# Kernel tuning notes

Measured on AMD Instinct MI355X. Metric: run time of the kernel, lower is better.

The kernel has to match this reference:

```python
import jax, jax.numpy as jnp
import numpy as np

B, IN_C, W, H = 16, 1024, 32, 32
P = 256          # planes
HEADS = 4
D = P // HEADS   # 64
N = W * H
EPS = 1e-6


def setup_inputs() -> dict:
    key = jax.random.key(0)
    ks = jax.random.split(key, 12)
    s = lambda fan_in: 1.0 / np.sqrt(fan_in)
    return {
        "x": jax.random.normal(ks[0], (B, IN_C, W, H), jnp.float32),
        "w_ds": jax.random.normal(ks[1], (P, IN_C), jnp.float32) * s(IN_C),
        "wq": jax.random.normal(ks[2], (P, P), jnp.float32) * s(P),
        "bq": jax.random.normal(ks[3], (P,), jnp.float32) * 0.01,
        "wk": jax.random.normal(ks[4], (P, P), jnp.float32) * s(P),
        "bk": jax.random.normal(ks[5], (P,), jnp.float32) * 0.01,
        "wv": jax.random.normal(ks[6], (P, P), jnp.float32) * s(P),
        "bv": jax.random.normal(ks[7], (P,), jnp.float32) * 0.01,
        "rel_h": jax.random.normal(ks[8], (1, HEADS, D, 1, H), jnp.float32),
        "rel_w": jax.random.normal(ks[9], (1, HEADS, D, W, 1), jnp.float32),
        "ln_w": jnp.ones((P,), jnp.float32),
        "ln_b": jnp.zeros((P,), jnp.float32),
        "w1": jax.random.normal(ks[10], (IN_C, P), jnp.float32) * s(P),
    }


def _conv1x1(w, x, b=None):
    # w: [out, in], x: [B, in, W, H]
    y = jnp.einsum('oc,bchw->bohw', w, x)
    if b is not None:
        y = y + b[None, :, None, None]
    return y


def reference(x, w_ds, wq, bq, wk, bk, wv, bv, rel_h, rel_w, ln_w, ln_b, w1):
    out = _conv1x1(w_ds, x)  # [B, P, W, H]

    # --- MHSA ---
    q = _conv1x1(wq, out, bq).reshape(B, HEADS, D, N)
    k = _conv1x1(wk, out, bk).reshape(B, HEADS, D, N)
    v = _conv1x1(wv, out, bv).reshape(B, HEADS, D, N)

    content_content = jnp.einsum('bhdi,bhdj->bhij', q, k)  # q^T k
    pos = (rel_h + rel_w).reshape(1, HEADS, D, N)           # [1,h,d,N]
    # content_position[i,j] = pos_i . q_j  (faithful to original: matmul with q)
    content_position = jnp.einsum('xhdi,bhdj->bhij', pos, q)
    attn = jax.nn.softmax(content_content + content_position, axis=-1)
    # out[.., d, i] = sum_j v[.., d, j] * attn[.., i, j]
    o = jnp.einsum('bhdj,bhij->bhdi', v, attn).reshape(B, P, W, H)

    # --- LayerNorm (channels_last over channel dim) ---
    y = o.transpose(0, 2, 3, 1)  # [B, W, H, P]
    mu = y.mean(-1, keepdims=True)
    var = ((y - mu) ** 2).mean(-1, keepdims=True)
    y = (y - mu) / jnp.sqrt(var + EPS) * ln_w + ln_b
    y = y.transpose(0, 3, 1, 2)  # [B, P, W, H]

    # --- expand conv + exact GELU + residual ---
    out2 = jax.nn.gelu(_conv1x1(w1, y), approximate=False)
    return out2 + x
```

## Files before the change

### kernel.cpp

```cpp
#include <hip/hip_runtime.h>
#include <hip/hip_bf16.h>
#include <math.h>

#define NN 1024
#define PP 256
#define INC 1024

typedef _Float16 f16_t;
typedef __attribute__((ext_vector_type(8))) _Float16 f16x8;
typedef __attribute__((ext_vector_type(4))) _Float16 f16x4;
typedef __attribute__((ext_vector_type(4))) float f32x4;
typedef __attribute__((ext_vector_type(16))) float f32x16;
typedef __attribute__((ext_vector_type(4))) int i32x4;

__device__ __forceinline__ float gelu_exact(float v) {
    return 0.5f * v * (1.0f + erff(v * 0.70710678118654752440f));
}

__device__ __forceinline__ void cvt_store(const float* __restrict__ s,
                                          f16_t* __restrict__ d, int j) {
    float4 v = ((const float4*)s)[j];
    f16x4 o = {(f16_t)v.x, (f16_t)v.y, (f16_t)v.z, (f16_t)v.w};
    ((f16x4*)d)[j] = o;
}

__global__ __launch_bounds__(256) void prep_k(
    const float* __restrict__ w_ds, const float* __restrict__ wq,
    const float* __restrict__ wk, const float* __restrict__ wv,
    const float* __restrict__ w1, const float* __restrict__ rel_h,
    const float* __restrict__ rel_w, const float* __restrict__ bq,
    const float* __restrict__ bk, const float* __restrict__ bv,
    f16_t* __restrict__ wdsh, f16_t* __restrict__ wqkv,
    f16_t* __restrict__ w1h, f16_t* __restrict__ post,
    float* __restrict__ bqkv)
{
    int i = blockIdx.x * 256 + threadIdx.x;
    if (i < 65536) {
        cvt_store(w_ds, wdsh, i);
    } else if (i < 81920) {
        cvt_store(wq, wqkv, i - 65536);
    } else if (i < 98304) {
        cvt_store(wk, wqkv + 65536, i - 81920);
    } else if (i < 114688) {
        cvt_store(wv, wqkv + 131072, i - 98304);
    } else if (i < 180224) {
        cvt_store(w1, w1h, i - 114688);
    } else if (i < 245760) {
        int j = i - 180224;
        int flat = j * 4;
        int d = flat & 63;
        int n = (flat >> 6) & 1023;
        int h = flat >> 16;
        f16x4 pk;
        #pragma unroll
        for (int jj = 0; jj < 4; ++jj) {
            float v = rel_h[(h * 64 + d + jj) * 32 + (n & 31)]
                    + rel_w[(h * 64 + d + jj) * 32 + (n >> 5)];
            pk[jj] = (f16_t)v;
        }
        *(f16x4*)&post[flat] = pk;
    } else if (i < 245952) {
        int j = i - 245760;
        int which = j >> 6, r = j & 63;
        const float* src = which == 0 ? bq : (which == 1 ? bk : bv);
        float4 v = ((const float4*)src)[r];
        ((float4*)bqkv)[which * 64 + r] = v;
    }
}

__global__ __launch_bounds__(256) void transpose_xk(const float* __restrict__ x,
                                                    f16_t* __restrict__ xt) {
    __shared__ float T[64][68];
    int tid = threadIdx.x;
    int n0 = blockIdx.x * 64, c0 = blockIdx.y * 64;
    size_t b = blockIdx.z;
    const float* xp = x + b * 1048576;
    int cl = tid >> 4, n4 = (tid & 15) * 4;
    #pragma unroll
    for (int it = 0; it < 4; ++it) {
        float4 v = *(const float4*)&xp[(size_t)(c0 + cl + it * 16) * 1024 + n0 + n4];
        *(float4*)&T[cl + it * 16][n4] = v;
    }
    __syncthreads();
    int nl = tid >> 3, ck = tid & 7;
    f16_t* xo = xt + b * 1048576;
    #pragma unroll
    for (int it = 0; it < 2; ++it) {
        int n = nl + it * 32;
        f16x8 pk;
        #pragma unroll
        for (int j = 0; j < 8; ++j) pk[j] = (f16_t)T[ck * 8 + j][n];
        *(f16x8*)&xo[(size_t)(n0 + n) * 1024 + c0 + ck * 8] = pk;
    }
}

__global__ __launch_bounds__(64) void hgemm(
    const f16_t* __restrict__ A, const f16_t* __restrict__ Bt,
    const float* __restrict__ bias, const float* __restrict__ resid,
    f16_t* __restrict__ Cq, f16_t* __restrict__ Ck, f16_t* __restrict__ Cv,
    float* __restrict__ Cf,
    int M, int N, int K, int mode)
{
    int l = threadIdx.x;
    int lo = l & 15, hi = l >> 4;
    int m0 = blockIdx.y * 64;
    int n0 = blockIdx.x * 32;
    size_t bb = blockIdx.z;

    const f16_t* Ap = A + (size_t)(m0 + lo) * K + hi * 8;
    const f16_t* Bq = Bt + bb * (size_t)N * K + (size_t)(n0 + lo) * K + hi * 8;

    f32x4 acc[4][2] = {};

    #pragma unroll 2
    for (int k0 = 0; k0 < K; k0 += 32) {
        f16x8 bfr0 = *(const f16x8*)(Bq + k0);
        f16x8 bfr1 = *(const f16x8*)(Bq + (size_t)16 * K + k0);
        #pragma unroll
        for (int fm = 0; fm < 4; ++fm) {
            f16x8 af = *(const f16x8*)(Ap + (size_t)fm * 16 * K + k0);
            acc[fm][0] = __builtin_amdgcn_mfma_f32_16x16x32_f16(af, bfr0, acc[fm][0], 0, 0, 0);
            acc[fm][1] = __builtin_amdgcn_mfma_f32_16x16x32_f16(af, bfr1, acc[fm][1], 0, 0, 0);
        }
    }

    #pragma unroll
    for (int fn = 0; fn < 2; ++fn) {
        int n = n0 + fn * 16 + lo;
        #pragma unroll
        for (int fm = 0; fm < 4; ++fm) {
            int mb = m0 + fm * 16 + hi * 4;
            f32x4 a = acc[fm][fn];
            if (mode == 0) {
                f16x4 st;
                #pragma unroll
                for (int r = 0; r < 4; ++r) st[r] = (f16_t)a[r];
                *(f16x4*)&Cq[((size_t)bb * N + n) * M + mb] = st;
            } else if (mode == 1) {
                int which = mb >> 8;
                int mloc = mb & 255;
                int hh = mloc >> 6, d0 = mloc & 63;
                if (which == 2) {
                    #pragma unroll
                    for (int r = 0; r < 4; ++r)
                        Cv[(((size_t)bb * 4 + hh) * 64 + d0 + r) * NN + n] = (f16_t)(a[r] + bias[mb + r]);
                } else {
                    f16_t* dst = which ? Ck : Cq;
                    f16x4 st;
                    #pragma unroll
                    for (int r = 0; r < 4; ++r) st[r] = (f16_t)(a[r] + bias[mb + r]);
                    *(f16x4*)&dst[(((size_t)bb * 4 + hh) * NN + n) * 64 + d0] = st;
                }
            } else {
                #pragma unroll
                for (int r = 0; r < 4; ++r) {
                    size_t idx = ((size_t)bb * M + mb + r) * N + n;
                    Cf[idx] = gelu_exact(a[r]) + resid[idx];
                }
            }
        }
    }
}

__global__ __launch_bounds__(64) void attn_mfma(
    const f16_t* __restrict__ q_t, const f16_t* __restrict__ k_t,
    const f16_t* __restrict__ v_b, const f16_t* __restrict__ pos_t,
    f16_t* __restrict__ o)
{
    int l = threadIdx.x;
    int lq = l & 31;
    int half = l >> 5;
    int h = blockIdx.y, b = blockIdx.z;
    int q0 = blockIdx.x * 32;
    size_t base = (size_t)(b * 4 + h) * (NN * 64);

    f16x8 Bq0, Bq1, Bq2, Bq3, Bq4, Bq5, Bq6, Bq7;
    {
        const f16_t* qr = q_t + base + (size_t)(q0 + lq) * 64 + half * 8;
        Bq0 = *(const f16x8*)(qr);
        Bq1 = *(const f16x8*)(qr + 16);
        Bq2 = *(const f16x8*)(qr + 32);
        Bq3 = *(const f16x8*)(qr + 48);
        const f16_t* pr = pos_t + ((size_t)h * NN + q0 + lq) * 64 + half * 8;
        Bq4 = *(const f16x8*)(pr);
        Bq5 = *(const f16x8*)(pr + 16);
        Bq6 = *(const f16x8*)(pr + 32);
        Bq7 = *(const f16x8*)(pr + 48);
    }

    f32x16 accD0 = {}, accD1 = {};
    float m_run = -1e30f, l_run = 0.0f;

    const f16_t* kbase = k_t + base + (size_t)lq * 64 + half * 8;
    const f16_t* qbase = q_t + base + (size_t)lq * 64 + half * 8;
    const f16_t* vbase = v_b + base + (size_t)lq * NN + half * 8;

    f16x8 aK0, aK1, aK2, aK3, aQ0, aQ1, aQ2, aQ3, aV00, aV01, aV10, aV11;
    f16x8 bK0, bK1, bK2, bK3, bQ0, bQ1, bQ2, bQ3, bV00, bV01, bV10, bV11;

#define LOADT(S, J) do { \
    const f16_t* ka_ = kbase + (size_t)(J) * 64; \
    S##K0 = *(const f16x8*)(ka_);       S##K1 = *(const f16x8*)(ka_ + 16); \
    S##K2 = *(const f16x8*)(ka_ + 32);  S##K3 = *(const f16x8*)(ka_ + 48); \
    const f16_t* qa_ = qbase + (size_t)(J) * 64; \
    S##Q0 = *(const f16x8*)(qa_);       S##Q1 = *(const f16x8*)(qa_ + 16); \
    S##Q2 = *(const f16x8*)(qa_ + 32);  S##Q3 = *(const f16x8*)(qa_ + 48); \
    const f16_t* va_ = vbase + (J); \
    S##V00 = *(const f16x8*)(va_);          S##V01 = *(const f16x8*)(va_ + 16); \
    S##V10 = *(const f16x8*)(va_ + 32 * NN); S##V11 = *(const f16x8*)(va_ + 32 * NN + 16); \
} while (0)

#define COMPUTE(S) do { \
    f32x16 sc = {}; \
    sc = __builtin_amdgcn_mfma_f32_32x32x16_f16(S##K0, Bq0, sc, 0, 0, 0); \
    sc = __builtin_amdgcn_mfma_f32_32x32x16_f16(S##K1, Bq1, sc, 0, 0, 0); \
    sc = __builtin_amdgcn_mfma_f32_32x32x16_f16(S##K2, Bq2, sc, 0, 0, 0); \
    sc = __builtin_amdgcn_mfma_f32_32x32x16_f16(S##K3, Bq3, sc, 0, 0, 0); \
    sc = __builtin_amdgcn_mfma_f32_32x32x16_f16(S##Q0, Bq4, sc, 0, 0, 0); \
    sc = __builtin_amdgcn_mfma_f32_32x32x16_f16(S##Q1, Bq5, sc, 0, 0, 0); \
    sc = __builtin_amdgcn_mfma_f32_32x32x16_f16(S##Q2, Bq6, sc, 0, 0, 0); \
    sc = __builtin_amdgcn_mfma_f32_32x32x16_f16(S##Q3, Bq7, sc, 0, 0, 0); \
    float mt = sc[0]; \
    _Pragma("unroll") \
    for (int r = 1; r < 16; ++r) mt = fmaxf(mt, sc[r]); \
    mt = fmaxf(mt, __shfl_xor(mt, 32, 64)); \
    if (!__all(mt <= m_run + 8.0f)) { \
        float mnew = fmaxf(m_run, mt); \
        float alpha = __expf(m_run - mnew); \
        m_run = mnew; l_run *= alpha; \
        _Pragma("unroll") \
        for (int r = 0; r < 16; ++r) { accD0[r] *= alpha; accD1[r] *= alpha; } \
    } \
    float p[16]; float rs = 0.0f; \
    _Pragma("unroll") \
    for (int r = 0; r < 16; ++r) { p[r] = __expf(sc[r] - m_run); rs += p[r]; } \
    rs += __shfl_xor(rs, 32, 64); \
    l_run += rs; \
    int w0 = __builtin_bit_cast(int, __builtin_amdgcn_cvt_pkrtz(p[0], p[1])); \
    int w1 = __builtin_bit_cast(int, __builtin_amdgcn_cvt_pkrtz(p[2], p[3])); \
    int w2 = __builtin_bit_cast(int, __builtin_amdgcn_cvt_pkrtz(p[4], p[5])); \
    int w3 = __builtin_bit_cast(int, __builtin_amdgcn_cvt_pkrtz(p[6], p[7])); \
    int w4 = __builtin_bit_cast(int, __builtin_amdgcn_cvt_pkrtz(p[8], p[9])); \
    int w5 = __builtin_bit_cast(int, __builtin_amdgcn_cvt_pkrtz(p[10], p[11])); \
    int w6 = __builtin_bit_cast(int, __builtin_amdgcn_cvt_pkrtz(p[12], p[13])); \
    int w7 = __builtin_bit_cast(int, __builtin_amdgcn_cvt_pkrtz(p[14], p[15])); \
    int x0 = __shfl_xor(w0, 32, 64), x1 = __shfl_xor(w1, 32, 64); \
    int x2 = __shfl_xor(w2, 32, 64), x3 = __shfl_xor(w3, 32, 64); \
    int x4 = __shfl_xor(w4, 32, 64), x5 = __shfl_xor(w5, 32, 64); \
    int x6 = __shfl_xor(w6, 32, 64), x7 = __shfl_xor(w7, 32, 64); \
    i32x4 pb0 = { half ? x2 : w0, half ? x3 : w1, half ? w2 : x0, half ? w3 : x1 }; \
    i32x4 pb1 = { half ? x6 : w4, half ? x7 : w5, half ? w6 : x4, half ? w7 : x5 }; \
    f16x8 Pf0 = __builtin_bit_cast(f16x8, pb0); \
    f16x8 Pf1 = __builtin_bit_cast(f16x8, pb1); \
    accD0 = __builtin_amdgcn_mfma_f32_32x32x16_f16(S##V00, Pf0, accD0, 0, 0, 0); \
    accD0 = __builtin_amdgcn_mfma_f32_32x32x16_f16(S##V01, Pf1, accD0, 0, 0, 0); \
    accD1 = __builtin_amdgcn_mfma_f32_32x32x16_f16(S##V10, Pf0, accD1, 0, 0, 0); \
    accD1 = __builtin_amdgcn_mfma_f32_32x32x16_f16(S##V11, Pf1, accD1, 0, 0, 0); \
} while (0)

    LOADT(a, 0);
    for (int t = 0; t < 32; t += 2) {
        LOADT(b, (t + 1) * 32);
        COMPUTE(a);
        LOADT(a, (size_t)(((t + 2) & 31) * 32));
        COMPUTE(b);
    }
#undef LOADT
#undef COMPUTE

    float inv = 1.0f / l_run;
    size_t orow = ((size_t)b * NN + q0 + lq) * 256 + h * 64;
    #pragma unroll
    for (int rg = 0; rg < 4; ++rg) {
        f16x4 s0, s1;
        #pragma unroll
        for (int c = 0; c < 4; ++c) {
            s0[c] = (f16_t)(accD0[rg * 4 + c] * inv);
            s1[c] = (f16_t)(accD1[rg * 4 + c] * inv);
        }
        *(f16x4*)&o[orow + rg * 8 + half * 4] = s0;
        *(f16x4*)&o[orow + 32 + rg * 8 + half * 4] = s1;
    }
}

__global__ __launch_bounds__(256) void ln_k(const f16_t* __restrict__ o,
                                            f16_t* __restrict__ yt,
                                            const float* __restrict__ lw,
                                            const float* __restrict__ lb)
{
    int tid = threadIdx.x;
    int wv = tid >> 6, l = tid & 63;
    size_t row = (size_t)blockIdx.x * 4 + wv;
    f16x4 v4 = ((const f16x4*)(o + row * 256))[l];
    float v[4];
    #pragma unroll
    for (int j = 0; j < 4; ++j) v[j] = (float)v4[j];
    float s = v[0] + v[1] + v[2] + v[3];
    float q = v[0]*v[0] + v[1]*v[1] + v[2]*v[2] + v[3]*v[3];
    #pragma unroll
    for (int off = 1; off < 64; off <<= 1) {
        s += __shfl_xor(s, off, 64);
        q += __shfl_xor(q, off, 64);
    }
    float mean = s * (1.0f / 256.0f);
    float var = q * (1.0f / 256.0f) - mean * mean;
    float rstd = rsqrtf(var + 1e-6f);
    f32x4 w4 = ((const f32x4*)lw)[l];
    f32x4 b4 = ((const f32x4*)lb)[l];
    f16x4 o4;
    #pragma unroll
    for (int j = 0; j < 4; ++j)
        o4[j] = (f16_t)((v[j] - mean) * rstd * w4[j] + b4[j]);
    ((f16x4*)(yt + row * 256))[l] = o4;
}

extern "C" void kernel_launch(void* const* d_in, const int* in_sizes, int n_in,
                              void* d_out, int out_size, void* d_ws, size_t ws_size,
                              hipStream_t stream) {
    const float* x     = (const float*)d_in[0];
    const float* w_ds  = (const float*)d_in[1];
    const float* wq    = (const float*)d_in[2];
    const float* bq    = (const float*)d_in[3];
    const float* wk    = (const float*)d_in[4];
    const float* bk    = (const float*)d_in[5];
    const float* wv    = (const float*)d_in[6];
    const float* bv    = (const float*)d_in[7];
    const float* rel_h = (const float*)d_in[8];
    const float* rel_w = (const float*)d_in[9];
    const float* ln_w  = (const float*)d_in[10];
    const float* ln_b  = (const float*)d_in[11];
    const float* w1    = (const float*)d_in[12];
    float* out = (float*)d_out;

    f16_t* xt    = (f16_t*)d_ws;
    f16_t* wdsh  = xt + 16777216;
    f16_t* wqkv  = wdsh + 262144;
    f16_t* w1h   = wqkv + 196608;
    f16_t* post  = w1h + 262144;
    f16_t* out0t = post + 262144;
    f16_t* qt    = out0t + 4194304;
    f16_t* kt    = qt + 4194304;
    f16_t* vb    = kt + 4194304;
    f16_t* ytb   = vb + 4194304;
    f16_t* oat   = ytb + 4194304;
    float* bqkv  = (float*)(oat + 4194304);

    prep_k<<<961, 256, 0, stream>>>(w_ds, wq, wk, wv, w1, rel_h, rel_w,
                                    bq, bk, bv, wdsh, wqkv, w1h, post, bqkv);
    transpose_xk<<<dim3(16, 16, 16), 256, 0, stream>>>(x, xt);

    hgemm<<<dim3(32, 4, 16), 64, 0, stream>>>(wdsh, xt, nullptr, nullptr,
                                              out0t, nullptr, nullptr, nullptr,
                                              PP, NN, INC, 0);
    hgemm<<<dim3(32, 12, 16), 64, 0, stream>>>(wqkv, out0t, bqkv, nullptr,
                                               qt, kt, vb, nullptr,
                                               768, NN, PP, 1);
    attn_mfma<<<dim3(32, 4, 16), 64, 0, stream>>>(qt, kt, vb, post, oat);
    ln_k<<<4096, 256, 0, stream>>>(oat, ytb, ln_w, ln_b);
    hgemm<<<dim3(32, 16, 16), 64, 0, stream>>>(w1h, ytb, nullptr, x,
                                               nullptr, nullptr, nullptr, out,
                                               INC, NN, PP, 3);
}
```

Baseline: 396.6 us.

## Split attention KV range across four waves and shrink GEMM M-tiles

The attention kernel now runs four waves per block. Each wave processes a quarter of the key/value sequence, and the partial softmax statistics and accumulators are merged through shared memory with a log-sum-exp rescale before one wave writes the output. This gives each block more parallelism and shortens the serial KV loop. The GEMM kernel is templated on M-fragment count, and the first two GEMMs use smaller M-tiles to launch more blocks. The cost is extra synchronisation and shared-memory traffic in attention, and less A/B reuse per block in the GEMMs.

New measurement: 529.3 us. +33.5%, slower.

```diff
diff --git a/kernel.cpp b/kernel.cpp
--- a/kernel.cpp
+++ b/kernel.cpp
@@ -94,6 +94,7 @@
     }
 }
 
+template<int MFR>
 __global__ __launch_bounds__(64) void hgemm(
     const f16_t* __restrict__ A, const f16_t* __restrict__ Bt,
     const float* __restrict__ bias, const float* __restrict__ resid,
@@ -103,21 +104,21 @@
 {
     int l = threadIdx.x;
     int lo = l & 15, hi = l >> 4;
-    int m0 = blockIdx.y * 64;
+    int m0 = blockIdx.y * (MFR * 16);
     int n0 = blockIdx.x * 32;
     size_t bb = blockIdx.z;
 
     const f16_t* Ap = A + (size_t)(m0 + lo) * K + hi * 8;
     const f16_t* Bq = Bt + bb * (size_t)N * K + (size_t)(n0 + lo) * K + hi * 8;
 
-    f32x4 acc[4][2] = {};
+    f32x4 acc[MFR][2] = {};
 
     #pragma unroll 2
     for (int k0 = 0; k0 < K; k0 += 32) {
         f16x8 bfr0 = *(const f16x8*)(Bq + k0);
         f16x8 bfr1 = *(const f16x8*)(Bq + (size_t)16 * K + k0);
         #pragma unroll
-        for (int fm = 0; fm < 4; ++fm) {
+        for (int fm = 0; fm < MFR; ++fm) {
             f16x8 af = *(const f16x8*)(Ap + (size_t)fm * 16 * K + k0);
             acc[fm][0] = __builtin_amdgcn_mfma_f32_16x16x32_f16(af, bfr0, acc[fm][0], 0, 0, 0);
             acc[fm][1] = __builtin_amdgcn_mfma_f32_16x16x32_f16(af, bfr1, acc[fm][1], 0, 0, 0);
@@ -128,7 +129,7 @@
     for (int fn = 0; fn < 2; ++fn) {
         int n = n0 + fn * 16 + lo;
         #pragma unroll
-        for (int fm = 0; fm < 4; ++fm) {
+        for (int fm = 0; fm < MFR; ++fm) {
             int mb = m0 + fm * 16 + hi * 4;
             f32x4 a = acc[fm][fn];
             if (mode == 0) {
@@ -162,12 +163,16 @@
     }
 }
 
-__global__ __launch_bounds__(64) void attn_mfma(
+__global__ __launch_bounds__(256, 4) void attn_mfma(
     const f16_t* __restrict__ q_t, const f16_t* __restrict__ k_t,
     const f16_t* __restrict__ v_b, const f16_t* __restrict__ pos_t,
     f16_t* __restrict__ o)
 {
-    int l = threadIdx.x;
+    __shared__ float cm[4][32], cl[4][32];
+    __shared__ __align__(16) float cacc[2][32][68];
+    int tid = threadIdx.x;
+    int wvi = tid >> 6;
+    int l = tid & 63;
     int lq = l & 31;
     int half = l >> 5;
     int h = blockIdx.y, b = blockIdx.z;
@@ -191,9 +196,9 @@
     f32x16 accD0 = {}, accD1 = {};
     float m_run = -1e30f, l_run = 0.0f;
 
-    const f16_t* kbase = k_t + base + (size_t)lq * 64 + half * 8;
-    const f16_t* qbase = q_t + base + (size_t)lq * 64 + half * 8;
-    const f16_t* vbase = v_b + base + (size_t)lq * NN + half * 8;
+    const f16_t* kbase = k_t + base + ((size_t)wvi * 256 + lq) * 64 + half * 8;
+    const f16_t* qabase = q_t + base + ((size_t)wvi * 256 + lq) * 64 + half * 8;
+    const f16_t* vbase = v_b + base + (size_t)lq * NN + wvi * 256 + half * 8;
 
     f16x8 aK0, aK1, aK2, aK3, aQ0, aQ1, aQ2, aQ3, aV00, aV01, aV10, aV11;
     f16x8 bK0, bK1, bK2, bK3, bQ0, bQ1, bQ2, bQ3, bV00, bV01, bV10, bV11;
@@ -202,7 +207,7 @@
     const f16_t* ka_ = kbase + (size_t)(J) * 64; \
     S##K0 = *(const f16x8*)(ka_);       S##K1 = *(const f16x8*)(ka_ + 16); \
     S##K2 = *(const f16x8*)(ka_ + 32);  S##K3 = *(const f16x8*)(ka_ + 48); \
-    const f16_t* qa_ = qbase + (size_t)(J) * 64; \
+    const f16_t* qa_ = qabase + (size_t)(J) * 64; \
     S##Q0 = *(const f16x8*)(qa_);       S##Q1 = *(const f16x8*)(qa_ + 16); \
     S##Q2 = *(const f16x8*)(qa_ + 32);  S##Q3 = *(const f16x8*)(qa_ + 48); \
     const f16_t* va_ = vbase + (J); \
@@ -259,27 +264,82 @@
 } while (0)
 
     LOADT(a, 0);
-    for (int t = 0; t < 32; t += 2) {
+    for (int t = 0; t < 8; t += 2) {
         LOADT(b, (t + 1) * 32);
         COMPUTE(a);
-        LOADT(a, (size_t)(((t + 2) & 31) * 32));
+        LOADT(a, ((t + 2) & 7) * 32);
         COMPUTE(b);
     }
 #undef LOADT
 #undef COMPUTE
 
-    float inv = 1.0f / l_run;
-    size_t orow = ((size_t)b * NN + q0 + lq) * 256 + h * 64;
-    #pragma unroll
-    for (int rg = 0; rg < 4; ++rg) {
-        f16x4 s0, s1;
-        #pragma unroll
-        for (int c = 0; c < 4; ++c) {
-            s0[c] = (f16_t)(accD0[rg * 4 + c] * inv);
-            s1[c] = (f16_t)(accD1[rg * 4 + c] * inv);
-        }
-        *(f16x4*)&o[orow + rg * 8 + half * 4] = s0;
-        *(f16x4*)&o[orow + 32 + rg * 8 + half * 4] = s1;
+    if (half == 0) { cm[wvi][lq] = m_run; cl[wvi][lq] = l_run; }
+    __syncthreads();
+    float m0v = cm[0][lq], m1v = cm[1][lq], m2v = cm[2][lq], m3v = cm[3][lq];
+    float mg = fmaxf(fmaxf(m0v, m1v), fmaxf(m2v, m3v));
+    float lg = cl[0][lq] * __expf(m0v - mg) + cl[1][lq] * __expf(m1v - mg)
+             + cl[2][lq] * __expf(m2v - mg) + cl[3][lq] * __expf(m3v - mg);
+    float alpha = __expf(m_run - mg);
+    #pragma unroll
+    for (int r = 0; r < 16; ++r) { accD0[r] *= alpha; accD1[r] *= alpha; }
+
+    if (wvi & 1) {
+        int bi = wvi >> 1;
+        #pragma unroll
+        for (int rg = 0; rg < 4; ++rg) {
+            int d0 = rg * 8 + half * 4;
+            float4 v0 = {accD0[rg*4+0], accD0[rg*4+1], accD0[rg*4+2], accD0[rg*4+3]};
+            float4 v1 = {accD1[rg*4+0], accD1[rg*4+1], accD1[rg*4+2], accD1[rg*4+3]};
+            *(float4*)&cacc[bi][lq][d0] = v0;
+            *(float4*)&cacc[bi][lq][32 + d0] = v1;
+        }
+    }
+    __syncthreads();
+    if (!(wvi & 1)) {
+        int bi = wvi >> 1;
+        #pragma unroll
+        for (int rg = 0; rg < 4; ++rg) {
+            int d0 = rg * 8 + half * 4;
+            float4 v0 = *(const float4*)&cacc[bi][lq][d0];
+            float4 v1 = *(const float4*)&cacc[bi][lq][32 + d0];
+            accD0[rg*4+0] += v0.x; accD0[rg*4+1] += v0.y; accD0[rg*4+2] += v0.z; accD0[rg*4+3] += v0.w;
+            accD1[rg*4+0] += v1.x; accD1[rg*4+1] += v1.y; accD1[rg*4+2] += v1.z; accD1[rg*4+3] += v1.w;
+        }
+    }
+    __syncthreads();
+    if (wvi == 2) {
+        #pragma unroll
+        for (int rg = 0; rg < 4; ++rg) {
+            int d0 = rg * 8 + half * 4;
+            float4 v0 = {accD0[rg*4+0], accD0[rg*4+1], accD0[rg*4+2], accD0[rg*4+3]};
+            float4 v1 = {accD1[rg*4+0], accD1[rg*4+1], accD1[rg*4+2], accD1[rg*4+3]};
+            *(float4*)&cacc[1][lq][d0] = v0;
+            *(float4*)&cacc[1][lq][32 + d0] = v1;
+        }
+    }
+    __syncthreads();
+    if (wvi == 0) {
+        #pragma unroll
+        for (int rg = 0; rg < 4; ++rg) {
+            int d0 = rg * 8 + half * 4;
+            float4 v0 = *(const float4*)&cacc[1][lq][d0];
+            float4 v1 = *(const float4*)&cacc[1][lq][32 + d0];
+            accD0[rg*4+0] += v0.x; accD0[rg*4+1] += v0.y; accD0[rg*4+2] += v0.z; accD0[rg*4+3] += v0.w;
+            accD1[rg*4+0] += v1.x; accD1[rg*4+1] += v1.y; accD1[rg*4+2] += v1.z; accD1[rg*4+3] += v1.w;
+        }
+        float inv = 1.0f / lg;
+        size_t orow = ((size_t)b * NN + q0 + lq) * 256 + h * 64;
+        #pragma unroll
+        for (int rg = 0; rg < 4; ++rg) {
+            f16x4 s0, s1;
+            #pragma unroll
+            for (int c = 0; c < 4; ++c) {
+                s0[c] = (f16_t)(accD0[rg * 4 + c] * inv);
+                s1[c] = (f16_t)(accD1[rg * 4 + c] * inv);
+            }
+            *(f16x4*)&o[orow + rg * 8 + half * 4] = s0;
+            *(f16x4*)&o[orow + 32 + rg * 8 + half * 4] = s1;
+        }
     }
 }
 
@@ -349,15 +409,15 @@
                                     bq, bk, bv, wdsh, wqkv, w1h, post, bqkv);
     transpose_xk<<<dim3(16, 16, 16), 256, 0, stream>>>(x, xt);
 
-    hgemm<<<dim3(32, 4, 16), 64, 0, stream>>>(wdsh, xt, nullptr, nullptr,
-                                              out0t, nullptr, nullptr, nullptr,
-                                              PP, NN, INC, 0);
-    hgemm<<<dim3(32, 12, 16), 64, 0, stream>>>(wqkv, out0t, bqkv, nullptr,
-                                               qt, kt, vb, nullptr,
-                                               768, NN, PP, 1);
-    attn_mfma<<<dim3(32, 4, 16), 64, 0, stream>>>(qt, kt, vb, post, oat);
+    hgemm<2><<<dim3(32, 8, 16), 64, 0, stream>>>(wdsh, xt, nullptr, nullptr,
+                                                 out0t, nullptr, nullptr, nullptr,
+                                                 PP, NN, INC, 0);
+    hgemm<2><<<dim3(32, 24, 16), 64, 0, stream>>>(wqkv, out0t, bqkv, nullptr,
+                                                  qt, kt, vb, nullptr,
+                                                  768, NN, PP, 1);
+    attn_mfma<<<dim3(32, 4, 16), 256, 0, stream>>>(qt, kt, vb, post, oat);
     ln_k<<<4096, 256, 0, stream>>>(oat, ytb, ln_w, ln_b);
-    hgemm<<<dim3(32, 16, 16), 64, 0, stream>>>(w1h, ytb, nullptr, x,
-                                               nullptr, nullptr, nullptr, out,
-                                               INC, NN, PP, 3);
-}
+    hgemm<4><<<dim3(32, 16, 16), 64, 0, stream>>>(w1h, ytb, nullptr, x,
+                                                  nullptr, nullptr, nullptr, out,
+                                                  INC, NN, PP, 3);
+}
```
